# Kernel tuning notes

Measured on AMD Instinct MI355X. Metric: run time of the kernel, lower is better.

Reference implementation:

```python
import jax, jax.numpy as jnp
import numpy as np

C_M = 256   # norm_channel (msa channel)
C_Z = 128   # pair_channel
H = 8       # num_head
C = 32      # attention_channel per head


def layer_norm(x, gamma, beta, eps=1e-5):
    mu = jnp.mean(x, axis=-1, keepdims=True)
    var = jnp.var(x, axis=-1, keepdims=True)
    return (x - mu) * jax.lax.rsqrt(var + eps) * gamma + beta


def setup_inputs() -> dict:
    key = jax.random.key(0)
    ks = jax.random.split(key, 12)
    B, S, R = 1, 128, 256
    inp = {
        "msa_act": jax.random.normal(ks[0], (B, S, R, C_M), jnp.float32),
        "pair_act": jax.random.normal(ks[1], (B, R, R, C_Z), jnp.float32),
        "msa_mask": jnp.ones((B, S, R), jnp.float32),
        # query_norm params
        "qn_g": jnp.ones((C_M,), jnp.float32),
        "qn_b": jnp.zeros((C_M,), jnp.float32),
        # feat_2d_norm params
        "pn_g": jnp.ones((C_Z,), jnp.float32),
        "pn_b": jnp.zeros((C_Z,), jnp.float32),
        # feat_2d_weights: Linear(C_Z -> H, bias=False)
        "w2d": jax.random.normal(ks[2], (C_Z, H), jnp.float32) / np.sqrt(C_Z),
        # attention projections [C_M, H, C]
        "wq": jax.random.normal(ks[3], (C_M, H, C), jnp.float32) / np.sqrt(C_M),
        "wk": jax.random.normal(ks[4], (C_M, H, C), jnp.float32) / np.sqrt(C_M),
        "wv": jax.random.normal(ks[5], (C_M, H, C), jnp.float32) / np.sqrt(C_M),
        # gating linear [C_M, H, C] + bias
        "wg": jax.random.normal(ks[6], (C_M, H, C), jnp.float32) / np.sqrt(C_M),
        "bg": jnp.ones((H, C), jnp.float32),
        # output linear [H, C, C_M] + bias
        "wo": jax.random.normal(ks[7], (H, C, C_M), jnp.float32) / np.sqrt(H * C),
        "bo": jnp.zeros((C_M,), jnp.float32),
    }
    return inp


def reference(msa_act, pair_act, msa_mask, qn_g, qn_b, pn_g, pn_b, w2d,
              wq, wk, wv, wg, bg, wo, bo):
    # Pair bias: LayerNorm -> Linear(C_Z->H) -> permute to [B, 1, H, R, R]
    z = layer_norm(pair_act, pn_g, pn_b)            # [B, R, R, C_Z]
    z = jnp.einsum('bqkc,ch->bhqk', z, w2d)          # [B, H, R, R]
    z = z[:, None]                                   # [B, 1, H, R, R]

    # Mask bias: [B, S, 1, 1, R]
    mask_bias = (1e9 * (msa_mask - 1.0))[:, :, None, None, :]

    # Row-wise MHA with query norm
    m = layer_norm(msa_act, qn_g, qn_b)              # [B, S, R, C_M]
    scale = 1.0 / np.sqrt(C)
    q = jnp.einsum('bsqc,chd->bshqd', m, wq) * scale
    k = jnp.einsum('bskc,chd->bshkd', m, wk)
    v = jnp.einsum('bskc,chd->bshkd', m, wv)

    logits = jnp.einsum('bshqd,bshkd->bshqk', q, k) + mask_bias + z
    a = jax.nn.softmax(logits, axis=-1)              # [B, S, H, R, R]
    o = jnp.einsum('bshqk,bshkd->bsqhd', a, v)       # [B, S, R, H, C]

    g = jax.nn.sigmoid(jnp.einsum('bsqc,chd->bsqhd', m, wg) + bg)
    o = o * g
    out = jnp.einsum('bsqhd,hdc->bsqc', o, wo) + bo  # [B, S, R, C_M]
    return out
```

## Files before the change

### kernel.cpp

```cpp
#include <hip/hip_runtime.h>
#include <hip/hip_bf16.h>

typedef unsigned short u16;
typedef __attribute__((ext_vector_type(8))) short bf16x8;
typedef __attribute__((ext_vector_type(4))) float f32x4;

__device__ __forceinline__ float bf2f(u16 u){
  union { unsigned int i; float f; } v; v.i = ((unsigned int)u) << 16; return v.f;
}
__device__ __forceinline__ u16 f2bf(float f){
  union { float f; unsigned int i; } v; v.f = f;
  unsigned int i = v.i;
  return (u16)((i + 0x7fffu + ((i >> 16) & 1u)) >> 16);
}
__device__ __forceinline__ unsigned int pk2(float a, float b){
  union { __hip_bfloat162 v; unsigned int u; } c;
  c.v = __float22bfloat162_rn(float2{a, b});
  return c.u;
}
__device__ __forceinline__ float ldin(const void* p, int i, int f){
  return f ? ((const float*)p)[i] : bf2f(((const u16*)p)[i]);
}
__device__ __forceinline__ bf16x8 pack8(const float* v){
  union { bf16x8 v8; unsigned int w[4]; } u;
  #pragma unroll
  for (int j = 0; j < 4; ++j) u.w[j] = pk2(v[2*j], v[2*j+1]);
  return u.v8;
}

__global__ void k_sniff(const unsigned int* __restrict__ msa_w, int* __restrict__ flag)
{
  int lane = threadIdx.x & 63;
  int lo0 = 0, expok = 0;
  #pragma unroll
  for (int j = 0; j < 4; ++j) {
    unsigned int w = msa_w[lane * 4 + j];
    if ((w & 0xffffu) == 0u) lo0++;
    unsigned int e = (w >> 7) & 0xffu;
    if (e >= 110u && e <= 140u) expok++;
  }
  #pragma unroll
  for (int off = 1; off < 64; off <<= 1) {
    lo0   += __shfl_xor(lo0,   off, 64);
    expok += __shfl_xor(expok, off, 64);
  }
  if (lane == 0 && blockIdx.x == 0)
    *flag = (lo0 > 200) ? 1 : ((expok > 200) ? 0 : 1);
}

__global__ __launch_bounds__(256) void k_transpose(
    const void* __restrict__ wq, const void* __restrict__ wk,
    const void* __restrict__ wv, const void* __restrict__ wg,
    const void* __restrict__ wo, const int* __restrict__ flagp,
    u16* __restrict__ Wt, u16* __restrict__ wot)
{
  __shared__ u16 T[64 * 72];
  const int flag = *flagp;
  const int t = threadIdx.x;
  const int mat = blockIdx.x >> 4, tile = blockIdx.x & 15;
  const int R0 = (tile >> 2) * 64, C0 = (tile & 3) * 64;
  const void* src = (mat == 0) ? wq : (mat == 1) ? wk : (mat == 2) ? wv
                  : (mat == 3) ? wg : wo;
  u16* dst = (mat < 4) ? (Wt + mat * 65536) : wot;
  {
    int i = t >> 2, j0 = (t & 3) * 16;
    #pragma unroll
    for (int e = 0; e < 8; ++e) {
      float a = ldin(src, (R0 + i) * 256 + C0 + j0 + 2*e,     flag);
      float b = ldin(src, (R0 + i) * 256 + C0 + j0 + 2*e + 1, flag);
      *(unsigned int*)(T + i * 72 + j0 + 2*e) = pk2(a, b);
    }
  }
  __syncthreads();
  {
    int j = t >> 2, i0 = (t & 3) * 16;
    u16 o[16];
    #pragma unroll
    for (int e = 0; e < 16; ++e) o[e] = T[(i0 + e) * 72 + j];
    *(uint4*)(dst + (C0 + j) * 256 + R0 + i0)     = *(const uint4*)o;
    *(uint4*)(dst + (C0 + j) * 256 + R0 + i0 + 8) = *(const uint4*)(o + 8);
  }
}

__global__ __launch_bounds__(256) void k_pair_z(
    const void* __restrict__ pair, const void* __restrict__ png,
    const void* __restrict__ pnb, const void* __restrict__ w2d,
    const int* __restrict__ flagp, u16* __restrict__ z_bf)
{
  __shared__ u16 As[64 * 136];
  __shared__ u16 Bs[16 * 136];
  const int flag = *flagp;
  const int t = threadIdx.x, lane = t & 63, wave = t >> 6;
  const int g = lane >> 4, l15 = lane & 15;
  const int rowBase = blockIdx.x * 64;

  if (t < 128) {
    #pragma unroll
    for (int n = 0; n < 16; ++n)
      Bs[n * 136 + t] = (n < 8) ? f2bf(ldin(w2d, t * 8 + n, flag)) : (u16)0;
  }
  {
    int lrow = t >> 2, cb = (t & 3) * 32;
    int base = (rowBase + lrow) * 128 + cb;
    float x[32];
    if (flag) {
      const float* p = (const float*)pair + base;
      #pragma unroll
      for (int j = 0; j < 8; ++j) {
        float4 f4 = *(const float4*)(p + 4 * j);
        x[4*j] = f4.x; x[4*j+1] = f4.y; x[4*j+2] = f4.z; x[4*j+3] = f4.w;
      }
    } else {
      const u16* p = (const u16*)pair + base;
      #pragma unroll
      for (int j = 0; j < 4; ++j) {
        uint4 u = *(const uint4*)(p + 8 * j);
        const u16* h = (const u16*)&u;
        #pragma unroll
        for (int e = 0; e < 8; ++e) x[8*j+e] = bf2f(h[e]);
      }
    }
    float s = 0.f, sq = 0.f;
    #pragma unroll
    for (int j = 0; j < 32; ++j) { s += x[j]; sq += x[j] * x[j]; }
    s  += __shfl_xor(s, 1, 64);  s  += __shfl_xor(s, 2, 64);
    sq += __shfl_xor(sq, 1, 64); sq += __shfl_xor(sq, 2, 64);
    float mu = s * (1.f / 128.f);
    float var = sq * (1.f / 128.f) - mu * mu;
    float rs = rsqrtf(var + 1e-5f);
    float n_[32];
    #pragma unroll
    for (int j = 0; j < 32; ++j) {
      int c = cb + j;
      n_[j] = (x[j] - mu) * rs * ldin(png, c, flag) + ldin(pnb, c, flag);
    }
    u16* dst = As + lrow * 136 + cb;
    #pragma unroll
    for (int j = 0; j < 16; ++j)
      *(unsigned int*)(dst + 2*j) = pk2(n_[2*j], n_[2*j+1]);
  }
  __syncthreads();

  f32x4 accz = {0.f, 0.f, 0.f, 0.f};
  #pragma unroll
  for (int kb = 0; kb < 4; ++kb) {
    bf16x8 a = *(const bf16x8*)(As + (wave * 16 + l15) * 136 + kb * 32 + g * 8);
    bf16x8 b = *(const bf16x8*)(Bs + l15 * 136 + kb * 32 + g * 8);
    accz = __builtin_amdgcn_mfma_f32_16x16x32_bf16(a, b, accz, 0, 0, 0);
  }
  if (l15 < 8) {
    #pragma unroll
    for (int r = 0; r < 4; ++r)
      z_bf[l15 * 65536 + rowBase + wave * 16 + g * 4 + r] = f2bf(accz[r]);
  }
}

__global__ __launch_bounds__(256) void k_msa_ln(
    const void* __restrict__ msa, const void* __restrict__ qng,
    const void* __restrict__ qnb, const int* __restrict__ flagp,
    u16* __restrict__ m_bf)
{
  const int flag = *flagp;
  int wave = threadIdx.x >> 6, lane = threadIdx.x & 63;
  int row = blockIdx.x * 4 + wave;
  float x[4];
  if (flag) {
    float4 f4 = *((const float4*)msa + row * 64 + lane);
    x[0]=f4.x; x[1]=f4.y; x[2]=f4.z; x[3]=f4.w;
  } else {
    uint2 u = *((const uint2*)msa + row * 64 + lane);
    const u16* h = (const u16*)&u;
    #pragma unroll
    for (int j = 0; j < 4; ++j) x[j] = bf2f(h[j]);
  }
  float s = 0.f, sq = 0.f;
  #pragma unroll
  for (int j = 0; j < 4; ++j) { s += x[j]; sq += x[j] * x[j]; }
  #pragma unroll
  for (int off = 1; off < 64; off <<= 1) {
    s  += __shfl_xor(s,  off, 64);
    sq += __shfl_xor(sq, off, 64);
  }
  float mu = s * (1.f / 256.f);
  float var = sq * (1.f / 256.f) - mu * mu;
  float rs = rsqrtf(var + 1e-5f);
  float y[4];
  #pragma unroll
  for (int j = 0; j < 4; ++j) {
    int c = lane * 4 + j;
    y[j] = (x[j] - mu) * rs * ldin(qng, c, flag) + ldin(qnb, c, flag);
  }
  uint2 o2;
  o2.x = pk2(y[0], y[1]);
  o2.y = pk2(y[2], y[3]);
  *((uint2*)m_bf + row * 64 + lane) = o2;
}

__global__ __launch_bounds__(256, 2) void k_fused(
    const u16* __restrict__ m_bf, const u16* __restrict__ Wt,
    const void* __restrict__ bg, const u16* __restrict__ z_bf,
    const void* __restrict__ mask, const int* __restrict__ flagp,
    u16* __restrict__ og_ws)
{
  __shared__ u16 Ks[256 * 40];
  __shared__ u16 Vts[32 * 264];
  __shared__ u16 Qs[4][64 * 40];
  __shared__ float Tb[4][16 * 36];
  __shared__ float Mb[256];
  const int flag = *flagp;
  const int t = threadIdx.x, lane = t & 63, wave = t >> 6;
  const int s_ = blockIdx.x, h = blockIdx.y;
  const int g = lane >> 4, l15 = lane & 15;

  Mb[t] = 1e9f * (ldin(mask, s_ * 256 + t, flag) - 1.0f);

  bf16x8 af[8][4];
  #pragma unroll
  for (int kb = 0; kb < 8; ++kb)
    #pragma unroll
    for (int mt = 0; mt < 4; ++mt)
      af[kb][mt] = *(const bf16x8*)(
          m_bf + (s_ * 256 + wave * 64 + mt * 16 + l15) * 256 + kb * 32 + g * 8);

  const float scale = 0.17677669529663687f;
  float gg[4][2][4];
  f32x4 zero = {0.f, 0.f, 0.f, 0.f};

  #pragma unroll
  for (int matid = 0; matid < 4; ++matid) {
    const u16* W = Wt + matid * 65536 + (h * 32) * 256;
    f32x4 acc[4][2];
    #pragma unroll
    for (int mt = 0; mt < 4; ++mt) { acc[mt][0] = zero; acc[mt][1] = zero; }
    #pragma unroll
    for (int kb = 0; kb < 8; ++kb) {
      bf16x8 b0 = *(const bf16x8*)(W + l15 * 256        + kb * 32 + g * 8);
      bf16x8 b1 = *(const bf16x8*)(W + (16 + l15) * 256 + kb * 32 + g * 8);
      #pragma unroll
      for (int mt = 0; mt < 4; ++mt) {
        acc[mt][0] = __builtin_amdgcn_mfma_f32_16x16x32_bf16(af[kb][mt], b0, acc[mt][0], 0, 0, 0);
        acc[mt][1] = __builtin_amdgcn_mfma_f32_16x16x32_bf16(af[kb][mt], b1, acc[mt][1], 0, 0, 0);
      }
    }
    #pragma unroll
    for (int mt = 0; mt < 4; ++mt)
      #pragma unroll
      for (int nt = 0; nt < 2; ++nt)
        #pragma unroll
        for (int r = 0; r < 4; ++r) {
          int rowl = wave * 64 + mt * 16 + g * 4 + r;
          int dd = nt * 16 + l15;
          float v = acc[mt][nt][r];
          if (matid == 0)
            Qs[wave][(mt * 16 + g * 4 + r) * 40 + dd] = f2bf(v * scale);
          else if (matid == 1)
            Ks[rowl * 40 + dd] = f2bf(v);
          else if (matid == 2)
            Vts[dd * 264 + rowl] = f2bf(v);
          else {
            float gv = v + ldin(bg, h * 32 + dd, flag);
            gg[mt][nt][r] = 1.0f / (1.0f + __expf(-gv));
          }
        }
  }
  __syncthreads();

  const u16* Qw = &Qs[wave][0];
  float* Tw = &Tb[wave][0];
  for (int qt = 0; qt < 4; ++qt) {
    const int qbase = wave * 64 + qt * 16;
    bf16x8 aq = *(const bf16x8*)(Qw + (qt * 16 + l15) * 40 + g * 8);
    f32x4 S[16];
    #pragma unroll
    for (int kt = 0; kt < 16; ++kt) {
      bf16x8 bk = *(const bf16x8*)(Ks + (kt * 16 + l15) * 40 + g * 8);
      S[kt] = __builtin_amdgcn_mfma_f32_16x16x32_bf16(aq, bk, zero, 0, 0, 0);
    }
    const u16* zb = z_bf + h * 65536 + (qbase + l15) * 256;
    uint4 zu[8];
    #pragma unroll
    for (int kc = 0; kc < 8; ++kc) zu[kc] = *(const uint4*)(zb + kc * 32 + g * 8);

    float L[8][8];
    #pragma unroll
    for (int kc = 0; kc < 8; ++kc) {
      asm volatile("s_waitcnt lgkmcnt(0)" ::: "memory");
      #pragma unroll
      for (int half = 0; half < 2; ++half)
        #pragma unroll
        for (int r = 0; r < 4; ++r)
          Tw[(g * 4 + r) * 36 + half * 16 + l15] = S[kc * 2 + half][r];
      asm volatile("s_waitcnt lgkmcnt(0)" ::: "memory");
      float4 t0 = *(const float4*)(Tw + l15 * 36 + g * 8);
      float4 t1 = *(const float4*)(Tw + l15 * 36 + g * 8 + 4);
      float4 m0 = *(const float4*)(Mb + kc * 32 + g * 8);
      float4 m1 = *(const float4*)(Mb + kc * 32 + g * 8 + 4);
      const u16* zh = (const u16*)&zu[kc];
      L[kc][0] = __expf(t0.x + m0.x + bf2f(zh[0]));
      L[kc][1] = __expf(t0.y + m0.y + bf2f(zh[1]));
      L[kc][2] = __expf(t0.z + m0.z + bf2f(zh[2]));
      L[kc][3] = __expf(t0.w + m0.w + bf2f(zh[3]));
      L[kc][4] = __expf(t1.x + m1.x + bf2f(zh[4]));
      L[kc][5] = __expf(t1.y + m1.y + bf2f(zh[5]));
      L[kc][6] = __expf(t1.z + m1.z + bf2f(zh[6]));
      L[kc][7] = __expf(t1.w + m1.w + bf2f(zh[7]));
    }
    float sm = 0.f;
    #pragma unroll
    for (int kc = 0; kc < 8; ++kc)
      #pragma unroll
      for (int j = 0; j < 8; ++j) sm += L[kc][j];
    sm += __shfl_xor(sm, 16, 64);
    sm += __shfl_xor(sm, 32, 64);
    f32x4 O0 = zero, O1 = zero;
    #pragma unroll
    for (int kc = 0; kc < 8; ++kc) {
      bf16x8 ap  = pack8(&L[kc][0]);
      bf16x8 bv0 = *(const bf16x8*)(Vts + l15 * 264 + kc * 32 + g * 8);
      bf16x8 bv1 = *(const bf16x8*)(Vts + (16 + l15) * 264 + kc * 32 + g * 8);
      O0 = __builtin_amdgcn_mfma_f32_16x16x32_bf16(ap, bv0, O0, 0, 0, 0);
      O1 = __builtin_amdgcn_mfma_f32_16x16x32_bf16(ap, bv1, O1, 0, 0, 0);
    }
    #pragma unroll
    for (int r = 0; r < 4; ++r) {
      float smr = __shfl(sm, g * 4 + r, 64);
      float inv = 1.0f / smr;
      int qq = qbase + g * 4 + r;
      int base = (s_ * 256 + qq) * 256 + h * 32;
      float o0 = O0[r] * inv * gg[qt][0][r];
      float o1 = O1[r] * inv * gg[qt][1][r];
      og_ws[base + l15]      = f2bf(o0);
      og_ws[base + 16 + l15] = f2bf(o1);
    }
  }
}

__global__ __launch_bounds__(256, 2) void k_outproj(
    const u16* __restrict__ og, const u16* __restrict__ wot,
    const void* __restrict__ bo, const int* __restrict__ flagp,
    void* __restrict__ outv)
{
  const int flag = *flagp;
  const int t = threadIdx.x, lane = t & 63, wave = t >> 6;
  const int wm = (wave >> 1) * 64, wn = (wave & 1) * 64;
  const int rowBase = blockIdx.x * 128;
  const int ct = blockIdx.y;
  const int g = lane >> 4, l15 = lane & 15;

  bf16x8 af[8][4];
  #pragma unroll
  for (int kb = 0; kb < 8; ++kb)
    #pragma unroll
    for (int mt = 0; mt < 4; ++mt)
      af[kb][mt] = *(const bf16x8*)(
          og + (rowBase + wm + mt * 16 + l15) * 256 + kb * 32 + g * 8);

  const u16* Wb = wot + (ct * 128 + wn) * 256;
  f32x4 acc[4][4];
  f32x4 zero = {0.f, 0.f, 0.f, 0.f};
  #pragma unroll
  for (int i = 0; i < 4; ++i)
    #pragma unroll
    for (int j = 0; j < 4; ++j) acc[i][j] = zero;
  #pragma unroll
  for (int kb = 0; kb < 8; ++kb) {
    bf16x8 bb[4];
    #pragma unroll
    for (int nt = 0; nt < 4; ++nt)
      bb[nt] = *(const bf16x8*)(Wb + (nt * 16 + l15) * 256 + kb * 32 + g * 8);
    #pragma unroll
    for (int mt = 0; mt < 4; ++mt)
      #pragma unroll
      for (int nt = 0; nt < 4; ++nt)
        acc[mt][nt] = __builtin_amdgcn_mfma_f32_16x16x32_bf16(
            af[kb][mt], bb[nt], acc[mt][nt], 0, 0, 0);
  }
  #pragma unroll
  for (int mt = 0; mt < 4; ++mt)
    #pragma unroll
    for (int nt = 0; nt < 4; ++nt)
      #pragma unroll
      for (int r = 0; r < 4; ++r) {
        int row = rowBase + wm + mt * 16 + g * 4 + r;
        int col = ct * 128 + wn + nt * 16 + l15;
        float val = acc[mt][nt][r] + ldin(bo, col, flag);
        if (flag) ((float*)outv)[row * 256 + col] = val;
        else      ((u16*)outv)[row * 256 + col]   = f2bf(val);
      }
}

extern "C" void kernel_launch(void* const* d_in, const int* in_sizes, int n_in,
                              void* d_out, int out_size, void* d_ws, size_t ws_size,
                              hipStream_t stream)
{
  const void* msa  = d_in[0];
  const void* pair = d_in[1];
  const void* mask = d_in[2];
  const void* qng  = d_in[3];
  const void* qnb  = d_in[4];
  const void* png  = d_in[5];
  const void* pnb  = d_in[6];
  const void* w2d  = d_in[7];
  const void* wq   = d_in[8];
  const void* wk   = d_in[9];
  const void* wv   = d_in[10];
  const void* wg   = d_in[11];
  const void* bg   = d_in[12];
  const void* wo   = d_in[13];
  const void* bo   = d_in[14];

  char* ws = (char*)d_ws;
  u16* z_bf  = (u16*)(ws + 0);
  u16* Wt    = (u16*)(ws + 1048576);
  u16* wot   = (u16*)(ws + 1572864);
  int* flag  = (int*)(ws + 1703936);
  u16* m_bf  = (u16*)(ws + 1704192);
  u16* og_ws = (u16*)(ws + 18481408);

  hipLaunchKernelGGL(k_sniff, dim3(1), dim3(64), 0, stream,
                     (const unsigned int*)msa, flag);
  hipLaunchKernelGGL(k_transpose, dim3(80), dim3(256), 0, stream,
                     wq, wk, wv, wg, wo, flag, Wt, wot);
  hipLaunchKernelGGL(k_msa_ln, dim3(8192), dim3(256), 0, stream,
                     msa, qng, qnb, flag, m_bf);
  hipLaunchKernelGGL(k_pair_z, dim3(1024), dim3(256), 0, stream,
                     pair, png, pnb, w2d, flag, z_bf);
  hipLaunchKernelGGL(k_fused, dim3(128, 8), dim3(256), 0, stream,
                     m_bf, Wt, bg, z_bf, mask, flag, og_ws);
  hipLaunchKernelGGL(k_outproj, dim3(256, 2), dim3(256), 0, stream,
                     og_ws, wot, bo, flag, d_out);
}
```

Baseline: 259.4 us.

## Restructure fused attention to keep Q in registers and stream softmax through MFMA

Q is now computed transposed so its MFMA output fragment can serve directly as the A operand of QK^T. This removes the Qs and Tb shared buffers and the shared-memory transpose of the logits. Softmax exponentials are packed straight into P fragments per 32-key chunk and fed to the PV MFMA, replacing the full 16x4 logit register array. The projections are split into K/V and Q/G passes that stream the m rows from global memory instead of holding all A fragments, which cuts registers and LDS so the launch bound can rise to three blocks per CU. The trade-off is that m is reloaded twice and the interleaved MFMA/exp chain has less independent work per step.

```diff
diff --git a/kernel.cpp b/kernel.cpp
--- a/kernel.cpp
+++ b/kernel.cpp
@@ -20,12 +20,6 @@
 }
 __device__ __forceinline__ float ldin(const void* p, int i, int f){
   return f ? ((const float*)p)[i] : bf2f(((const u16*)p)[i]);
-}
-__device__ __forceinline__ bf16x8 pack8(const float* v){
-  union { bf16x8 v8; unsigned int w[4]; } u;
-  #pragma unroll
-  for (int j = 0; j < 4; ++j) u.w[j] = pk2(v[2*j], v[2*j+1]);
-  return u.v8;
 }
 
 __global__ void k_sniff(const unsigned int* __restrict__ msa_w, int* __restrict__ flag)
@@ -196,7 +190,7 @@
   *((uint2*)m_bf + row * 64 + lane) = o2;
 }
 
-__global__ __launch_bounds__(256, 2) void k_fused(
+__global__ __launch_bounds__(256, 3) void k_fused(
     const u16* __restrict__ m_bf, const u16* __restrict__ Wt,
     const void* __restrict__ bg, const u16* __restrict__ z_bf,
     const void* __restrict__ mask, const int* __restrict__ flagp,
@@ -204,8 +198,6 @@
 {
   __shared__ u16 Ks[256 * 40];
   __shared__ u16 Vts[32 * 264];
-  __shared__ u16 Qs[4][64 * 40];
-  __shared__ float Tb[4][16 * 36];
   __shared__ float Mb[256];
   const int flag = *flagp;
   const int t = threadIdx.x, lane = t & 63, wave = t >> 6;
@@ -214,123 +206,156 @@
 
   Mb[t] = 1e9f * (ldin(mask, s_ * 256 + t, flag) - 1.0f);
 
-  bf16x8 af[8][4];
-  #pragma unroll
-  for (int kb = 0; kb < 8; ++kb)
+  const float scale = 0.17677669529663687f;
+  f32x4 zero = {0.f, 0.f, 0.f, 0.f};
+  const u16* mrow = m_bf + (s_ * 256 + wave * 64) * 256;
+
+  {
+    const u16* WK = Wt + 1 * 65536 + (h * 32) * 256;
+    const u16* WV = Wt + 2 * 65536 + (h * 32) * 256;
+    f32x4 ak[4][2], av[4][2];
+    #pragma unroll
+    for (int mt = 0; mt < 4; ++mt) {
+      ak[mt][0] = zero; ak[mt][1] = zero;
+      av[mt][0] = zero; av[mt][1] = zero;
+    }
+    #pragma unroll
+    for (int kb = 0; kb < 8; ++kb) {
+      bf16x8 a[4];
+      #pragma unroll
+      for (int mt = 0; mt < 4; ++mt)
+        a[mt] = *(const bf16x8*)(mrow + (mt * 16 + l15) * 256 + kb * 32 + g * 8);
+      bf16x8 k0 = *(const bf16x8*)(WK + l15 * 256        + kb * 32 + g * 8);
+      bf16x8 k1 = *(const bf16x8*)(WK + (16 + l15) * 256 + kb * 32 + g * 8);
+      bf16x8 v0 = *(const bf16x8*)(WV + l15 * 256        + kb * 32 + g * 8);
+      bf16x8 v1 = *(const bf16x8*)(WV + (16 + l15) * 256 + kb * 32 + g * 8);
+      #pragma unroll
+      for (int mt = 0; mt < 4; ++mt) {
+        ak[mt][0] = __builtin_amdgcn_mfma_f32_16x16x32_bf16(a[mt], k0, ak[mt][0], 0, 0, 0);
+        ak[mt][1] = __builtin_amdgcn_mfma_f32_16x16x32_bf16(a[mt], k1, ak[mt][1], 0, 0, 0);
+        av[mt][0] = __builtin_amdgcn_mfma_f32_16x16x32_bf16(a[mt], v0, av[mt][0], 0, 0, 0);
+        av[mt][1] = __builtin_amdgcn_mfma_f32_16x16x32_bf16(a[mt], v1, av[mt][1], 0, 0, 0);
+      }
+    }
     #pragma unroll
     for (int mt = 0; mt < 4; ++mt)
-      af[kb][mt] = *(const bf16x8*)(
-          m_bf + (s_ * 256 + wave * 64 + mt * 16 + l15) * 256 + kb * 32 + g * 8);
-
-  const float scale = 0.17677669529663687f;
+      #pragma unroll
+      for (int r = 0; r < 4; ++r) {
+        int rowl = wave * 64 + mt * 16 + g * 4 + r;
+        union { unsigned int u; u16 h2[2]; } kw, vw;
+        kw.u = pk2(ak[mt][0][r], ak[mt][1][r]);
+        vw.u = pk2(av[mt][0][r], av[mt][1][r]);
+        Ks[rowl * 40 + l15]          = kw.h2[0];
+        Ks[rowl * 40 + 16 + l15]     = kw.h2[1];
+        Vts[l15 * 264 + rowl]        = vw.h2[0];
+        Vts[(16 + l15) * 264 + rowl] = vw.h2[1];
+      }
+  }
+
+  unsigned int qp[4][4];
   float gg[4][2][4];
-  f32x4 zero = {0.f, 0.f, 0.f, 0.f};
-
-  #pragma unroll
-  for (int matid = 0; matid < 4; ++matid) {
-    const u16* W = Wt + matid * 65536 + (h * 32) * 256;
-    f32x4 acc[4][2];
-    #pragma unroll
-    for (int mt = 0; mt < 4; ++mt) { acc[mt][0] = zero; acc[mt][1] = zero; }
+  {
+    const u16* WQ = Wt + 0 * 65536 + (h * 32) * 256;
+    const u16* WG = Wt + 3 * 65536 + (h * 32) * 256;
+    f32x4 aq[4][2], ag[4][2];
+    #pragma unroll
+    for (int mt = 0; mt < 4; ++mt) {
+      aq[mt][0] = zero; aq[mt][1] = zero;
+      ag[mt][0] = zero; ag[mt][1] = zero;
+    }
     #pragma unroll
     for (int kb = 0; kb < 8; ++kb) {
-      bf16x8 b0 = *(const bf16x8*)(W + l15 * 256        + kb * 32 + g * 8);
-      bf16x8 b1 = *(const bf16x8*)(W + (16 + l15) * 256 + kb * 32 + g * 8);
+      bf16x8 a[4];
+      #pragma unroll
+      for (int mt = 0; mt < 4; ++mt)
+        a[mt] = *(const bf16x8*)(mrow + (mt * 16 + l15) * 256 + kb * 32 + g * 8);
+      bf16x8 q0 = *(const bf16x8*)(WQ + l15 * 256        + kb * 32 + g * 8);
+      bf16x8 q1 = *(const bf16x8*)(WQ + (16 + l15) * 256 + kb * 32 + g * 8);
+      bf16x8 g0 = *(const bf16x8*)(WG + l15 * 256        + kb * 32 + g * 8);
+      bf16x8 g1 = *(const bf16x8*)(WG + (16 + l15) * 256 + kb * 32 + g * 8);
       #pragma unroll
       for (int mt = 0; mt < 4; ++mt) {
-        acc[mt][0] = __builtin_amdgcn_mfma_f32_16x16x32_bf16(af[kb][mt], b0, acc[mt][0], 0, 0, 0);
-        acc[mt][1] = __builtin_amdgcn_mfma_f32_16x16x32_bf16(af[kb][mt], b1, acc[mt][1], 0, 0, 0);
-      }
-    }
-    #pragma unroll
-    for (int mt = 0; mt < 4; ++mt)
+        aq[mt][0] = __builtin_amdgcn_mfma_f32_16x16x32_bf16(q0, a[mt], aq[mt][0], 0, 0, 0);
+        aq[mt][1] = __builtin_amdgcn_mfma_f32_16x16x32_bf16(q1, a[mt], aq[mt][1], 0, 0, 0);
+        ag[mt][0] = __builtin_amdgcn_mfma_f32_16x16x32_bf16(a[mt], g0, ag[mt][0], 0, 0, 0);
+        ag[mt][1] = __builtin_amdgcn_mfma_f32_16x16x32_bf16(a[mt], g1, ag[mt][1], 0, 0, 0);
+      }
+    }
+    #pragma unroll
+    for (int mt = 0; mt < 4; ++mt) {
+      qp[mt][0] = pk2(aq[mt][0][0] * scale, aq[mt][0][1] * scale);
+      qp[mt][1] = pk2(aq[mt][0][2] * scale, aq[mt][0][3] * scale);
+      qp[mt][2] = pk2(aq[mt][1][0] * scale, aq[mt][1][1] * scale);
+      qp[mt][3] = pk2(aq[mt][1][2] * scale, aq[mt][1][3] * scale);
       #pragma unroll
       for (int nt = 0; nt < 2; ++nt)
         #pragma unroll
         for (int r = 0; r < 4; ++r) {
-          int rowl = wave * 64 + mt * 16 + g * 4 + r;
-          int dd = nt * 16 + l15;
-          float v = acc[mt][nt][r];
-          if (matid == 0)
-            Qs[wave][(mt * 16 + g * 4 + r) * 40 + dd] = f2bf(v * scale);
-          else if (matid == 1)
-            Ks[rowl * 40 + dd] = f2bf(v);
-          else if (matid == 2)
-            Vts[dd * 264 + rowl] = f2bf(v);
-          else {
-            float gv = v + ldin(bg, h * 32 + dd, flag);
-            gg[mt][nt][r] = 1.0f / (1.0f + __expf(-gv));
-          }
+          float gv = ag[mt][nt][r] + ldin(bg, h * 32 + nt * 16 + l15, flag);
+          gg[mt][nt][r] = 1.0f / (1.0f + __expf(-gv));
         }
+    }
   }
   __syncthreads();
 
-  const u16* Qw = &Qs[wave][0];
-  float* Tw = &Tb[wave][0];
+  #pragma unroll
   for (int qt = 0; qt < 4; ++qt) {
     const int qbase = wave * 64 + qt * 16;
-    bf16x8 aq = *(const bf16x8*)(Qw + (qt * 16 + l15) * 40 + g * 8);
-    f32x4 S[16];
-    #pragma unroll
-    for (int kt = 0; kt < 16; ++kt) {
-      bf16x8 bk = *(const bf16x8*)(Ks + (kt * 16 + l15) * 40 + g * 8);
-      S[kt] = __builtin_amdgcn_mfma_f32_16x16x32_bf16(aq, bk, zero, 0, 0, 0);
-    }
     const u16* zb = z_bf + h * 65536 + (qbase + l15) * 256;
-    uint4 zu[8];
-    #pragma unroll
-    for (int kc = 0; kc < 8; ++kc) zu[kc] = *(const uint4*)(zb + kc * 32 + g * 8);
-
-    float L[8][8];
+    uint2 zu[16];
+    #pragma unroll
+    for (int kt = 0; kt < 16; ++kt)
+      zu[kt] = *(const uint2*)(zb + kt * 16 + g * 4);
+
+    union { bf16x8 v; unsigned int w[4]; } aq;
+    aq.w[0] = qp[qt][0]; aq.w[1] = qp[qt][1];
+    aq.w[2] = qp[qt][2]; aq.w[3] = qp[qt][3];
+
+    float sm = 0.f;
+    f32x4 O0 = zero, O1 = zero;
     #pragma unroll
     for (int kc = 0; kc < 8; ++kc) {
-      asm volatile("s_waitcnt lgkmcnt(0)" ::: "memory");
-      #pragma unroll
-      for (int half = 0; half < 2; ++half)
-        #pragma unroll
-        for (int r = 0; r < 4; ++r)
-          Tw[(g * 4 + r) * 36 + half * 16 + l15] = S[kc * 2 + half][r];
-      asm volatile("s_waitcnt lgkmcnt(0)" ::: "memory");
-      float4 t0 = *(const float4*)(Tw + l15 * 36 + g * 8);
-      float4 t1 = *(const float4*)(Tw + l15 * 36 + g * 8 + 4);
-      float4 m0 = *(const float4*)(Mb + kc * 32 + g * 8);
-      float4 m1 = *(const float4*)(Mb + kc * 32 + g * 8 + 4);
-      const u16* zh = (const u16*)&zu[kc];
-      L[kc][0] = __expf(t0.x + m0.x + bf2f(zh[0]));
-      L[kc][1] = __expf(t0.y + m0.y + bf2f(zh[1]));
-      L[kc][2] = __expf(t0.z + m0.z + bf2f(zh[2]));
-      L[kc][3] = __expf(t0.w + m0.w + bf2f(zh[3]));
-      L[kc][4] = __expf(t1.x + m1.x + bf2f(zh[4]));
-      L[kc][5] = __expf(t1.y + m1.y + bf2f(zh[5]));
-      L[kc][6] = __expf(t1.z + m1.z + bf2f(zh[6]));
-      L[kc][7] = __expf(t1.w + m1.w + bf2f(zh[7]));
-    }
-    float sm = 0.f;
-    #pragma unroll
-    for (int kc = 0; kc < 8; ++kc)
-      #pragma unroll
-      for (int j = 0; j < 8; ++j) sm += L[kc][j];
+      unsigned int pw[4];
+      #pragma unroll
+      for (int half = 0; half < 2; ++half) {
+        const int kt = kc * 2 + half;
+        union { bf16x8 v; uint2 u2[2]; } kf;
+        const u16* kr = Ks + (kt * 16 + l15) * 40;
+        kf.u2[0] = *(const uint2*)(kr + g * 4);
+        kf.u2[1] = *(const uint2*)(kr + 16 + g * 4);
+        f32x4 S = __builtin_amdgcn_mfma_f32_16x16x32_bf16(kf.v, aq.v, zero, 0, 0, 0);
+        float4 mb = *(const float4*)(Mb + kt * 16 + g * 4);
+        const u16* zh = (const u16*)&zu[kt];
+        float e0 = __expf(S[0] + mb.x + bf2f(zh[0]));
+        float e1 = __expf(S[1] + mb.y + bf2f(zh[1]));
+        float e2 = __expf(S[2] + mb.z + bf2f(zh[2]));
+        float e3 = __expf(S[3] + mb.w + bf2f(zh[3]));
+        sm += (e0 + e1) + (e2 + e3);
+        pw[half * 2]     = pk2(e0, e1);
+        pw[half * 2 + 1] = pk2(e2, e3);
+      }
+      union { bf16x8 v; unsigned int w[4]; } pf;
+      pf.w[0] = pw[0]; pf.w[1] = pw[1]; pf.w[2] = pw[2]; pf.w[3] = pw[3];
+      union { bf16x8 v; uint2 u2[2]; } vf0, vf1;
+      const u16* vr0 = Vts + l15 * 264 + kc * 32;
+      const u16* vr1 = Vts + (16 + l15) * 264 + kc * 32;
+      vf0.u2[0] = *(const uint2*)(vr0 + g * 4);
+      vf0.u2[1] = *(const uint2*)(vr0 + 16 + g * 4);
+      vf1.u2[0] = *(const uint2*)(vr1 + g * 4);
+      vf1.u2[1] = *(const uint2*)(vr1 + 16 + g * 4);
+      O0 = __builtin_amdgcn_mfma_f32_16x16x32_bf16(pf.v, vf0.v, O0, 0, 0, 0);
+      O1 = __builtin_amdgcn_mfma_f32_16x16x32_bf16(pf.v, vf1.v, O1, 0, 0, 0);
+    }
     sm += __shfl_xor(sm, 16, 64);
     sm += __shfl_xor(sm, 32, 64);
-    f32x4 O0 = zero, O1 = zero;
-    #pragma unroll
-    for (int kc = 0; kc < 8; ++kc) {
-      bf16x8 ap  = pack8(&L[kc][0]);
-      bf16x8 bv0 = *(const bf16x8*)(Vts + l15 * 264 + kc * 32 + g * 8);
-      bf16x8 bv1 = *(const bf16x8*)(Vts + (16 + l15) * 264 + kc * 32 + g * 8);
-      O0 = __builtin_amdgcn_mfma_f32_16x16x32_bf16(ap, bv0, O0, 0, 0, 0);
-      O1 = __builtin_amdgcn_mfma_f32_16x16x32_bf16(ap, bv1, O1, 0, 0, 0);
-    }
     #pragma unroll
     for (int r = 0; r < 4; ++r) {
       float smr = __shfl(sm, g * 4 + r, 64);
       float inv = 1.0f / smr;
       int qq = qbase + g * 4 + r;
       int base = (s_ * 256 + qq) * 256 + h * 32;
-      float o0 = O0[r] * inv * gg[qt][0][r];
-      float o1 = O1[r] * inv * gg[qt][1][r];
-      og_ws[base + l15]      = f2bf(o0);
-      og_ws[base + 16 + l15] = f2bf(o1);
+      og_ws[base + l15]      = f2bf(O0[r] * inv * gg[qt][0][r]);
+      og_ws[base + 16 + l15] = f2bf(O1[r] * inv * gg[qt][1][r]);
     }
   }
 }
```

Result: slower. 443.0 us (+70.8%).
